# Optimization experiments

Measured on AMD Instinct MI355X. Metric: run time of the kernel, lower is better.

Reference implementation:

```python
import jax, jax.numpy as jnp
import numpy as np
import math

N_NODES = 50000
N_EDGES = 640000
IN_FEATS = 128
HEADS = 8
OUT_FEATS = 16
D_FF = 4 * IN_FEATS


def setup_inputs() -> dict:
    key = jax.random.key(0)
    ks = jax.random.split(key, 10)
    s = 0.05
    return {
        "feat": jax.random.normal(ks[0], (N_NODES, IN_FEATS), jnp.float32),
        "src": jax.random.randint(ks[1], (N_EDGES,), 0, N_NODES, jnp.int32),
        "dst": jax.random.randint(ks[2], (N_EDGES,), 0, N_NODES, jnp.int32),
        "Wq": jax.random.normal(ks[3], (IN_FEATS, HEADS * OUT_FEATS), jnp.float32) * s,
        "Wk": jax.random.normal(ks[4], (IN_FEATS, HEADS * OUT_FEATS), jnp.float32) * s,
        "Wv": jax.random.normal(ks[5], (IN_FEATS, HEADS * OUT_FEATS), jnp.float32) * s,
        "ln1_g": jnp.ones((IN_FEATS,), jnp.float32),
        "ln1_b": jnp.zeros((IN_FEATS,), jnp.float32),
        "W1": jax.random.normal(ks[6], (IN_FEATS, D_FF), jnp.float32) * s,
        "b1": jnp.zeros((D_FF,), jnp.float32),
        "prelu_a": jnp.full((D_FF,), 0.25, jnp.float32),  # torch PReLU default init
        "W2": jax.random.normal(ks[7], (D_FF, IN_FEATS), jnp.float32) * s,
        "b2": jnp.zeros((IN_FEATS,), jnp.float32),
    }


def layer_norm(x, g, b, eps=1e-5):
    mu = jnp.mean(x, axis=-1, keepdims=True)
    var = jnp.mean(jnp.square(x - mu), axis=-1, keepdims=True)
    return (x - mu) * jax.lax.rsqrt(var + eps) * g + b


def reference(feat, src, dst, Wq, Wk, Wv, ln1_g, ln1_b, W1, b1, prelu_a, W2, b2):
    N = feat.shape[0]
    feat_c = jax.lax.stop_gradient(feat)  # feat.clone().detach()
    q = (feat @ Wq).reshape(N, HEADS, OUT_FEATS)
    k = (feat_c @ Wk).reshape(N, HEADS, OUT_FEATS)
    v = (feat_c @ Wv).reshape(N, HEADS, OUT_FEATS)

    # edge score: dot(k[src], q[dst]) per head -> [E, H]
    e = jnp.einsum('ehd,ehd->eh', k[src], q[dst]) / math.sqrt(OUT_FEATS * HEADS)

    # segment softmax over incoming edges of each dst node
    m = jax.ops.segment_max(e, dst, num_segments=N)          # [N, H]
    e_exp = jnp.exp(e - m[dst])                              # [E, H]
    denom = jax.ops.segment_sum(e_exp, dst, num_segments=N)  # [N, H]
    a = e_exp / denom[dst]                                   # [E, H]

    # weighted scatter-sum aggregation
    msg = v[src] * a[:, :, None]                             # [E, H, D]
    ft2 = jax.ops.segment_sum(msg, dst, num_segments=N)      # [N, H, D]

    rst = ft2.reshape(feat.shape) + feat
    # NOTE: original applies ln1 twice (ln2 is unused) -- reproduced faithfully
    rst = layer_norm(rst, ln1_g, ln1_b)
    h = rst @ W1 + b1
    h = jnp.where(h >= 0, h, prelu_a * h)                    # PReLU, per-channel
    ffn = h @ W2 + b2
    rst = layer_norm(rst + ffn, ln1_g, ln1_b)
    return rst
```

## Files before the change

kernel.cpp:

```cpp
#include <hip/hip_runtime.h>

#define N_NODES 50000
#define N_EDGES 640000
#define F 128
#define DFF 512
#define NB 196

using u32 = unsigned int;
using u16 = unsigned short;

typedef __bf16 bf16x8 __attribute__((ext_vector_type(8)));
typedef float f32x4 __attribute__((ext_vector_type(4)));
typedef float f32x2 __attribute__((ext_vector_type(2)));

__device__ __forceinline__ float bf2f(u16 u) {
    return __uint_as_float(((u32)u) << 16);
}
__device__ __forceinline__ float blo(u32 p) { return __uint_as_float(p << 16); }
__device__ __forceinline__ float bhi(u32 p) { return __uint_as_float(p & 0xffff0000u); }
__device__ __forceinline__ u16 f2bf(float f) {
    u32 u = __float_as_uint(f);
    u += 0x7fffu + ((u >> 16) & 1u);
    return (u16)(u >> 16);
}
__device__ __forceinline__ u32 pack2(float a, float b) {
    return (u32)f2bf(a) | ((u32)f2bf(b) << 16);
}

#define FEAT_UNITS (N_NODES * F / 4)
#define PH_TOTAL (FEAT_UNITS + 180224 + N_EDGES)
__global__ void k_prep(const float* __restrict__ feat, u16* __restrict__ featb,
                       const float* __restrict__ Wq, const float* __restrict__ Wk,
                       const float* __restrict__ Wv, const float* __restrict__ W1,
                       const float* __restrict__ W2, u16* __restrict__ WT,
                       const int* __restrict__ dst, int* __restrict__ cnt) {
    int idx = blockIdx.x * 256 + threadIdx.x;
    if (idx < FEAT_UNITS) {
        float4 v = reinterpret_cast<const float4*>(feat)[idx];
        uint2 p;
        p.x = pack2(v.x, v.y);
        p.y = pack2(v.z, v.w);
        reinterpret_cast<uint2*>(featb)[idx] = p;
        return;
    }
    int wi = idx - FEAT_UNITS;
    if (wi < 180224) {
        if (wi < 49152) {
            int mi = wi >> 14;
            int local = wi & 16383;
            const float* W = (mi == 0) ? Wq : ((mi == 1) ? Wk : Wv);
            int n = local >> 7, k = local & 127;
            WT[wi] = f2bf(W[(size_t)k * 128 + n]);
        } else if (wi < 114688) {
            int local = wi - 49152;
            int n = local >> 7, k = local & 127;
            WT[wi] = f2bf(W1[(size_t)k * 512 + n]);
        } else {
            int local = wi - 114688;
            int n = local >> 9, k = local & 511;
            WT[wi] = f2bf(W2[(size_t)k * 128 + n]);
        }
        return;
    }
    int e = wi - 180224;
    if (e < N_EDGES) atomicAdd(&cnt[dst[e]], 1);
}

__global__ void k_bsum(const int* __restrict__ counts, int* __restrict__ bsum) {
    int i = blockIdx.x * 256 + threadIdx.x;
    int v = (i < N_NODES) ? counts[i] : 0;
#pragma unroll
    for (int off = 32; off >= 1; off >>= 1) v += __shfl_xor(v, off, 64);
    __shared__ int ws[4];
    int lane = threadIdx.x & 63, wid = threadIdx.x >> 6;
    if (lane == 0) ws[wid] = v;
    __syncthreads();
    if (threadIdx.x == 0) bsum[blockIdx.x] = ws[0] + ws[1] + ws[2] + ws[3];
}

__global__ void k_bfill(const int* __restrict__ counts, const int* __restrict__ bsum,
                        int* __restrict__ row_ptr) {
    int b = blockIdx.x, t = threadIdx.x;
    int lane = t & 63, wid = t >> 6;
    __shared__ int ws[4];
    __shared__ int sboff[256];

    int bv = (t < NB) ? bsum[t] : 0;
    int bincl = bv;
#pragma unroll
    for (int off = 1; off < 64; off <<= 1) {
        int u = __shfl_up(bincl, off, 64);
        if (lane >= off) bincl += u;
    }
    if (lane == 63) ws[wid] = bincl;
    __syncthreads();
    int bwo = 0;
#pragma unroll
    for (int j = 0; j < 4; ++j) if (j < wid) bwo += ws[j];
    sboff[t] = bwo + bincl - bv;
    __syncthreads();
    const int boff = sboff[b];

    int i = b * 256 + t;
    int v = (i < N_NODES) ? counts[i] : 0;
    int incl = v;
#pragma unroll
    for (int off = 1; off < 64; off <<= 1) {
        int u = __shfl_up(incl, off, 64);
        if (lane >= off) incl += u;
    }
    if (lane == 63) ws[wid] = incl;
    __syncthreads();
    int wo = 0;
#pragma unroll
    for (int j = 0; j < 4; ++j) if (j < wid) wo += ws[j];
    if (i < N_NODES) row_ptr[i] = boff + wo + incl - v;
    if (i == 0) row_ptr[N_NODES] = N_EDGES;
}

__global__ void k_fill(const int* __restrict__ src, const int* __restrict__ dst,
                       const int* __restrict__ row_ptr, int* __restrict__ fill,
                       int* __restrict__ csr_src) {
    int e = blockIdx.x * 256 + threadIdx.x;
    if (e < N_EDGES) {
        int d = dst[e];
        int pos = row_ptr[d] + atomicAdd(&fill[d], 1);
        csr_src[pos] = src[e];
    }
}

template <int EPI>
__global__ __launch_bounds__(256) void k_mm(
    const u16* __restrict__ A, int lda,
    const u16* __restrict__ BT,
    void* __restrict__ Cv, int ldc,
    int K,
    const float* __restrict__ bias,
    const float* __restrict__ prelu,
    const u16* __restrict__ resid,
    const float* __restrict__ g,
    const float* __restrict__ bb)
{
    __shared__ u16 smem[17408];
    u16* sA = smem;
    u16* sB = smem + 128 * 64;
    u16* sC = smem;

    const int t = threadIdx.x;
    const int w = t >> 6;
    const int lane = t & 63;
    const int ln = lane & 15, q4 = lane >> 4;
    const int row0 = blockIdx.x * 128;
    const int cb = blockIdx.y * 128;

    f32x4 acc[2][8];
#pragma unroll
    for (int mt = 0; mt < 2; ++mt)
#pragma unroll
        for (int nt = 0; nt < 8; ++nt)
            acc[mt][nt] = (f32x4){0.f, 0.f, 0.f, 0.f};

    uint4 pa[4], pb[4];
#define LOAD_A(kc)                                                             \
    {                                                                          \
        _Pragma("unroll") for (int i = 0; i < 4; ++i) {                        \
            int u = i * 256 + t, r = u >> 3, k8 = (u & 7) * 8;                 \
            int row = row0 + r;                                                \
            uint4 val = make_uint4(0, 0, 0, 0);                                \
            if (row < N_NODES)                                                 \
                val = *reinterpret_cast<const uint4*>(A + (size_t)row * lda + (kc) + k8); \
            pa[i] = val;                                                       \
        }                                                                      \
    }
#define LOAD_B(kc)                                                             \
    {                                                                          \
        _Pragma("unroll") for (int i = 0; i < 4; ++i) {                        \
            int u = i * 256 + t, r = u >> 3, k8 = (u & 7) * 8;                 \
            pb[i] = *reinterpret_cast<const uint4*>(BT + (size_t)(cb + r) * K + (kc) + k8); \
        }                                                                      \
    }

    LOAD_A(0);
    LOAD_B(0);

    for (int kc = 0; kc < K; kc += 64) {
#pragma unroll
        for (int i = 0; i < 4; ++i) {
            int u = i * 256 + t, r = u >> 3, gi = u & 7;
            int off = (r * 8 + (gi ^ (r & 7))) * 8;
            *reinterpret_cast<uint4*>(&sA[off]) = pa[i];
            *reinterpret_cast<uint4*>(&sB[off]) = pb[i];
        }
        __syncthreads();
        if (kc + 64 < K) {
            LOAD_A(kc + 64);
            LOAD_B(kc + 64);
        }
#pragma unroll
        for (int ks = 0; ks < 2; ++ks) {
            const int gsw = ks * 4 + q4;
            const int rA0 = w * 32 + ln;
            const int rA1 = rA0 + 16;
            bf16x8 a0 = *reinterpret_cast<const bf16x8*>(&sA[(rA0 * 8 + (gsw ^ (rA0 & 7))) * 8]);
            bf16x8 a1 = *reinterpret_cast<const bf16x8*>(&sA[(rA1 * 8 + (gsw ^ (rA1 & 7))) * 8]);
#pragma unroll
            for (int nt = 0; nt < 8; ++nt) {
                const int rB = nt * 16 + ln;
                bf16x8 b = *reinterpret_cast<const bf16x8*>(&sB[(rB * 8 + (gsw ^ (rB & 7))) * 8]);
                acc[0][nt] = __builtin_amdgcn_mfma_f32_16x16x32_bf16(a0, b, acc[0][nt], 0, 0, 0);
                acc[1][nt] = __builtin_amdgcn_mfma_f32_16x16x32_bf16(a1, b, acc[1][nt], 0, 0, 0);
            }
        }
        __syncthreads();
    }
#undef LOAD_A
#undef LOAD_B

    if (EPI == 0 || EPI == 1) {
        float bs[8], pr[8];
        if (EPI == 1) {
#pragma unroll
            for (int nt = 0; nt < 8; ++nt) {
                int col = cb + nt * 16 + ln;
                bs[nt] = bias[col];
                pr[nt] = prelu[col];
            }
        }
#pragma unroll
        for (int mt = 0; mt < 2; ++mt)
#pragma unroll
            for (int nt = 0; nt < 8; ++nt)
#pragma unroll
                for (int j = 0; j < 4; ++j) {
                    float x = acc[mt][nt][j];
                    if (EPI == 1) {
                        x += bs[nt];
                        x = (x >= 0.f) ? x : pr[nt] * x;
                    }
                    sC[(w * 32 + mt * 16 + q4 * 4 + j) * 136 + nt * 16 + ln] = f2bf(x);
                }
        __syncthreads();
        if (EPI == 0 && cb != 0) {
            u16* C = (u16*)Cv;
            const u32 vflag = (cb == 256) ? 1u : 0u;
#pragma unroll
            for (int i = 0; i < 32; ++i) {
                int u = i * 256 + t;
                int r = u >> 6, p = u & 63;
                int row = row0 + r;
                if (row < N_NODES) {
                    u32 pair = *reinterpret_cast<const u32*>(&sC[r * 136 + p * 2]);
                    int packed = __builtin_amdgcn_cvt_pk_fp8_f32(blo(pair), bhi(pair), 0, false);
                    C[(u32)row * 256u + 128u + (u32)p * 2u + vflag] = (u16)(packed & 0xffff);
                }
            }
        } else {
            u16* C = (u16*)Cv;
#pragma unroll
            for (int i = 0; i < 8; ++i) {
                int u = i * 256 + t;
                int r = u >> 4, c8 = (u & 15) * 8;
                int row = row0 + r;
                if (row < N_NODES) {
                    uint4 val = *reinterpret_cast<const uint4*>(&sC[r * 136 + c8]);
                    *reinterpret_cast<uint4*>(&C[(size_t)row * ldc + cb + c8]) = val;
                }
            }
        }
    } else {
        float* C = (float*)Cv;
        float bs[8], gv[8], bv[8];
#pragma unroll
        for (int nt = 0; nt < 8; ++nt) {
            int col = nt * 16 + ln;
            bs[nt] = bias[col];
            gv[nt] = g[col];
            bv[nt] = bb[col];
        }
#pragma unroll
        for (int mt = 0; mt < 2; ++mt)
#pragma unroll
            for (int j = 0; j < 4; ++j) {
                int row = row0 + w * 32 + mt * 16 + q4 * 4 + j;
                bool ok = row < N_NODES;
                float vals[8];
                float s = 0.f, ss = 0.f;
#pragma unroll
                for (int nt = 0; nt < 8; ++nt) {
                    float x = acc[mt][nt][j] + bs[nt];
                    if (ok) x += bf2f(resid[(size_t)row * 128 + nt * 16 + ln]);
                    vals[nt] = x;
                    s += x; ss += x * x;
                }
                s += __shfl_xor(s, 8, 16); ss += __shfl_xor(ss, 8, 16);
                s += __shfl_xor(s, 4, 16); ss += __shfl_xor(ss, 4, 16);
                s += __shfl_xor(s, 2, 16); ss += __shfl_xor(ss, 2, 16);
                s += __shfl_xor(s, 1, 16); ss += __shfl_xor(ss, 1, 16);
                float mu = s * (1.f / 128.f);
                float var = ss * (1.f / 128.f) - mu * mu;
                float rs = rsqrtf(var + 1e-5f);
                if (ok) {
#pragma unroll
                    for (int nt = 0; nt < 8; ++nt)
                        C[(size_t)row * 128 + nt * 16 + ln] =
                            (vals[nt] - mu) * rs * gv[nt] + bv[nt];
                }
            }
    }
}

__global__ __launch_bounds__(256) void k_attn(
    const u32* __restrict__ Q32, const float* __restrict__ feat,
    const int* __restrict__ row_ptr, const int* __restrict__ csr_src,
    const float* __restrict__ g, const float* __restrict__ bb,
    u16* __restrict__ rstb)
{
    const int w = threadIdx.x >> 6;
    const int lane = threadIdx.x & 63;
    const int n = blockIdx.x * 4 + w;
    if (n >= N_NODES) return;
    const float scale = 0.08838834764831845f;

    const u32 qp = Q32[(u32)n * 128u + (u32)lane];
    const float q0 = blo(qp), q1 = bhi(qp);
    const int e0 = row_ptr[n], e1 = row_ptr[n + 1];
    const u32 kvlane = 64u + (u32)lane;

    float l = 0.f, a0 = 0.f, a1 = 0.f;

#define LD4(S, KV)                                                                      \
    {                                                                                   \
        KV[0] = Q32[(u32)(S).x * 128u + kvlane];                                        \
        KV[1] = Q32[(u32)(S).y * 128u + kvlane];                                        \
        KV[2] = Q32[(u32)(S).z * 128u + kvlane];                                        \
        KV[3] = Q32[(u32)(S).w * 128u + kvlane];                                        \
    }
#define CG(KV)                                                                          \
    {                                                                                   \
        f32x2 k0 = __builtin_amdgcn_cvt_pk_f32_fp8((int)KV[0], false);                  \
        f32x2 k1 = __builtin_amdgcn_cvt_pk_f32_fp8((int)KV[1], false);                  \
        f32x2 k2 = __builtin_amdgcn_cvt_pk_f32_fp8((int)KV[2], false);                  \
        f32x2 k3 = __builtin_amdgcn_cvt_pk_f32_fp8((int)KV[3], false);                  \
        float p0 = k0.x * q0 + k0.y * q1;                                               \
        float p1 = k1.x * q0 + k1.y * q1;                                               \
        float p2 = k2.x * q0 + k2.y * q1;                                               \
        float p3 = k3.x * q0 + k3.y * q1;                                               \
        p0 += __shfl_xor(p0, 4, 8); p1 += __shfl_xor(p1, 4, 8);                         \
        p2 += __shfl_xor(p2, 4, 8); p3 += __shfl_xor(p3, 4, 8);                         \
        p0 += __shfl_xor(p0, 2, 8); p1 += __shfl_xor(p1, 2, 8);                         \
        p2 += __shfl_xor(p2, 2, 8); p3 += __shfl_xor(p3, 2, 8);                         \
        p0 += __shfl_xor(p0, 1, 8); p1 += __shfl_xor(p1, 1, 8);                         \
        p2 += __shfl_xor(p2, 1, 8); p3 += __shfl_xor(p3, 1, 8);                         \
        float ea = __expf(p0 * scale), eb = __expf(p1 * scale);                         \
        float ec = __expf(p2 * scale), ed = __expf(p3 * scale);                         \
        l += (ea + eb) + (ec + ed);                                                     \
        f32x2 v0 = __builtin_amdgcn_cvt_pk_f32_fp8((int)KV[0], true);                   \
        f32x2 v1 = __builtin_amdgcn_cvt_pk_f32_fp8((int)KV[1], true);                   \
        f32x2 v2 = __builtin_amdgcn_cvt_pk_f32_fp8((int)KV[2], true);                   \
        f32x2 v3 = __builtin_amdgcn_cvt_pk_f32_fp8((int)KV[3], true);                   \
        a0 += ea * v0.x + eb * v1.x + ec * v2.x + ed * v3.x;                            \
        a1 += ea * v0.y + eb * v1.y + ec * v2.y + ed * v3.y;                            \
    }

    int e = e0;
    int rem = e1 - e0;
    {
        int4 sA, sB;
        u32 kvA[4], kvB[4];
        if (rem >= 4) {
            sA = *reinterpret_cast<const int4*>(csr_src + e);
            LD4(sA, kvA);
            if (rem >= 8) {
                sB = *reinterpret_cast<const int4*>(csr_src + e + 4);
                while (true) {
                    if (rem >= 12) sA = *reinterpret_cast<const int4*>(csr_src + e + 8);
                    LD4(sB, kvB);
                    CG(kvA);
                    e += 4; rem -= 4;
                    if (rem < 8) { CG(kvB); e += 4; rem -= 4; break; }
                    if (rem >= 12) sB = *reinterpret_cast<const int4*>(csr_src + e + 8);
                    LD4(sA, kvA);
                    CG(kvB);
                    e += 4; rem -= 4;
                    if (rem < 8) { CG(kvA); e += 4; rem -= 4; break; }
                }
            } else {
                CG(kvA);
                e += 4; rem -= 4;
            }
        }
    }
    for (; e < e1; ++e) {
        int s0 = csr_src[e];
        u32 kv = Q32[(u32)s0 * 128u + kvlane];
        f32x2 kf = __builtin_amdgcn_cvt_pk_f32_fp8((int)kv, false);
        float p0 = kf.x * q0 + kf.y * q1;
        p0 += __shfl_xor(p0, 4, 8);
        p0 += __shfl_xor(p0, 2, 8);
        p0 += __shfl_xor(p0, 1, 8);
        float ea = __expf(p0 * scale);
        f32x2 vf = __builtin_amdgcn_cvt_pk_f32_fp8((int)kv, true);
        l += ea;
        a0 += ea * vf.x;
        a1 += ea * vf.y;
    }
#undef LD4
#undef CG

    float inv = (l > 0.f) ? 1.f / l : 0.f;
    const int c2 = lane * 2;
    const float2 fr = *reinterpret_cast<const float2*>(feat + (size_t)n * 128 + c2);
    float x0 = a0 * inv + fr.x;
    float x1 = a1 * inv + fr.y;

    float sum = x0 + x1, sq = x0 * x0 + x1 * x1;
#pragma unroll
    for (int off = 32; off >= 1; off >>= 1) {
        sum += __shfl_xor(sum, off, 64);
        sq += __shfl_xor(sq, off, 64);
    }
    float mu = sum * (1.f / 128.f);
    float var = sq * (1.f / 128.f) - mu * mu;
    float rs = rsqrtf(var + 1e-5f);
    float y0 = (x0 - mu) * rs * g[c2] + bb[c2];
    float y1 = (x1 - mu) * rs * g[c2 + 1] + bb[c2 + 1];
    reinterpret_cast<u32*>(rstb)[(size_t)n * 64 + lane] = pack2(y0, y1);
}

extern "C" void kernel_launch(void* const* d_in, const int* in_sizes, int n_in,
                              void* d_out, int out_size, void* d_ws, size_t ws_size,
                              hipStream_t stream)
{
    const float* feat = (const float*)d_in[0];
    const int* src    = (const int*)d_in[1];
    const int* dst    = (const int*)d_in[2];
    const float* Wq   = (const float*)d_in[3];
    const float* Wk   = (const float*)d_in[4];
    const float* Wv   = (const float*)d_in[5];
    const float* ln_g = (const float*)d_in[6];
    const float* ln_b = (const float*)d_in[7];
    const float* W1   = (const float*)d_in[8];
    const float* b1   = (const float*)d_in[9];
    const float* pa   = (const float*)d_in[10];
    const float* W2   = (const float*)d_in[11];
    const float* b2   = (const float*)d_in[12];

    u16* qkv   = (u16*)d_ws;
    u16* h     = qkv + (size_t)N_NODES * 384;
    u16* featb = h;
    u16* rstb  = h + (size_t)N_NODES * 512;
    u16* WT    = rstb + (size_t)N_NODES * 128;
    u16* BqkvT = WT;
    u16* W1T   = WT + 49152;
    u16* W2T   = WT + 114688;
    int* counts  = (int*)(WT + 180224);
    int* fill    = counts + N_NODES;
    int* row_ptr = fill + N_NODES;
    int* csr_src = row_ptr + N_NODES + 1;
    int* bsum    = csr_src + N_EDGES;

    hipMemsetAsync(counts, 0, sizeof(int) * 2 * N_NODES, stream);
    k_prep<<<(PH_TOTAL + 255) / 256, 256, 0, stream>>>(
        feat, featb, Wq, Wk, Wv, W1, W2, WT, dst, counts);

    k_bsum<<<NB, 256, 0, stream>>>(counts, bsum);
    k_bfill<<<NB, 256, 0, stream>>>(counts, bsum, row_ptr);
    k_fill<<<(N_EDGES + 255) / 256, 256, 0, stream>>>(src, dst, row_ptr, fill, csr_src);

    const int MBK = (N_NODES + 127) / 128;

    dim3 gqkv(MBK, 3);
    k_mm<0><<<gqkv, 256, 0, stream>>>(featb, 128, BqkvT, qkv, 256, 128,
                                      nullptr, nullptr, nullptr, nullptr, nullptr);

    k_attn<<<(N_NODES + 3) / 4, 256, 0, stream>>>((const u32*)qkv, feat, row_ptr, csr_src,
                                                  ln_g, ln_b, rstb);

    dim3 gf1(MBK, 4);
    k_mm<1><<<gf1, 256, 0, stream>>>(rstb, 128, W1T, h, 512, 128,
                                     b1, pa, nullptr, nullptr, nullptr);

    dim3 gf2(MBK, 1);
    k_mm<2><<<gf2, 256, 0, stream>>>(h, 512, W2T, d_out, 128, 512,
                                     b2, nullptr, rstb, ln_g, ln_b);
}
```

Baseline: 304.2 us.

## Fuse FFN GEMMs into one kernel keeping hidden activations in shared memory

```diff
diff --git a/kernel.cpp b/kernel.cpp
--- a/kernel.cpp
+++ b/kernel.cpp
@@ -216,16 +216,7 @@
 #undef LOAD_A
 #undef LOAD_B
 
-    if (EPI == 0 || EPI == 1) {
-        float bs[8], pr[8];
-        if (EPI == 1) {
-#pragma unroll
-            for (int nt = 0; nt < 8; ++nt) {
-                int col = cb + nt * 16 + ln;
-                bs[nt] = bias[col];
-                pr[nt] = prelu[col];
-            }
-        }
+    {
 #pragma unroll
         for (int mt = 0; mt < 2; ++mt)
 #pragma unroll
@@ -233,10 +224,6 @@
 #pragma unroll
                 for (int j = 0; j < 4; ++j) {
                     float x = acc[mt][nt][j];
-                    if (EPI == 1) {
-                        x += bs[nt];
-                        x = (x >= 0.f) ? x : pr[nt] * x;
-                    }
                     sC[(w * 32 + mt * 16 + q4 * 4 + j) * 136 + nt * 16 + ln] = f2bf(x);
                 }
         __syncthreads();
@@ -267,46 +254,141 @@
                 }
             }
         }
-    } else {
-        float* C = (float*)Cv;
-        float bs[8], gv[8], bv[8];
-#pragma unroll
-        for (int nt = 0; nt < 8; ++nt) {
-            int col = nt * 16 + ln;
-            bs[nt] = bias[col];
-            gv[nt] = g[col];
-            bv[nt] = bb[col];
-        }
+    }
+}
+
+__global__ __launch_bounds__(256) void k_ffn(
+    const u16* __restrict__ rstb,
+    const u16* __restrict__ W1T,
+    const u16* __restrict__ W2T,
+    const float* __restrict__ b1,
+    const float* __restrict__ prelu,
+    const float* __restrict__ b2,
+    const float* __restrict__ g,
+    const float* __restrict__ bb,
+    float* __restrict__ out)
+{
+    __shared__ u16 sA[16384];
+    __shared__ u16 sH[16384];
+
+    const int t = threadIdx.x;
+    const int w = t >> 6;
+    const int lane = t & 63;
+    const int ln = lane & 15, q4 = lane >> 4;
+    const int row0 = blockIdx.x * 128;
+
+#pragma unroll
+    for (int i = 0; i < 8; ++i) {
+        int u = i * 256 + t, r = u >> 4, gi = u & 15;
+        int row = row0 + r;
+        uint4 val = make_uint4(0, 0, 0, 0);
+        if (row < N_NODES)
+            val = *reinterpret_cast<const uint4*>(rstb + (size_t)row * 128 + gi * 8);
+        *reinterpret_cast<uint4*>(&sA[(r * 16 + (gi ^ (r & 15))) * 8]) = val;
+    }
+    __syncthreads();
+
+    const int rA0 = w * 32 + ln;
+    const int rA1 = rA0 + 16;
+
+    f32x4 acc2[2][8];
+#pragma unroll
+    for (int mt = 0; mt < 2; ++mt)
+#pragma unroll
+        for (int nt = 0; nt < 8; ++nt)
+            acc2[mt][nt] = (f32x4){0.f, 0.f, 0.f, 0.f};
+
+    for (int c = 0; c < 4; ++c) {
+        f32x4 acc1[2][8];
 #pragma unroll
         for (int mt = 0; mt < 2; ++mt)
 #pragma unroll
-            for (int j = 0; j < 4; ++j) {
-                int row = row0 + w * 32 + mt * 16 + q4 * 4 + j;
-                bool ok = row < N_NODES;
-                float vals[8];
-                float s = 0.f, ss = 0.f;
-#pragma unroll
-                for (int nt = 0; nt < 8; ++nt) {
-                    float x = acc[mt][nt][j] + bs[nt];
-                    if (ok) x += bf2f(resid[(size_t)row * 128 + nt * 16 + ln]);
-                    vals[nt] = x;
-                    s += x; ss += x * x;
+            for (int nt = 0; nt < 8; ++nt)
+                acc1[mt][nt] = (f32x4){0.f, 0.f, 0.f, 0.f};
+#pragma unroll
+        for (int ks = 0; ks < 4; ++ks) {
+            const int gsw = ks * 4 + q4;
+            bf16x8 a0 = *reinterpret_cast<const bf16x8*>(&sA[(rA0 * 16 + (gsw ^ (rA0 & 15))) * 8]);
+            bf16x8 a1 = *reinterpret_cast<const bf16x8*>(&sA[(rA1 * 16 + (gsw ^ (rA1 & 15))) * 8]);
+#pragma unroll
+            for (int nt = 0; nt < 8; ++nt) {
+                bf16x8 b = *reinterpret_cast<const bf16x8*>(
+                    W1T + (size_t)(c * 128 + nt * 16 + ln) * 128 + ks * 32 + q4 * 8);
+                acc1[0][nt] = __builtin_amdgcn_mfma_f32_16x16x32_bf16(a0, b, acc1[0][nt], 0, 0, 0);
+                acc1[1][nt] = __builtin_amdgcn_mfma_f32_16x16x32_bf16(a1, b, acc1[1][nt], 0, 0, 0);
+            }
+        }
+#pragma unroll
+        for (int mt = 0; mt < 2; ++mt)
+#pragma unroll
+            for (int nt = 0; nt < 8; ++nt) {
+                const int col = nt * 16 + ln;
+                const float bsv = b1[c * 128 + col];
+                const float prv = prelu[c * 128 + col];
+                const int gi = col >> 3;
+#pragma unroll
+                for (int j = 0; j < 4; ++j) {
+                    float x = acc1[mt][nt][j] + bsv;
+                    x = (x >= 0.f) ? x : prv * x;
+                    const int row = w * 32 + mt * 16 + q4 * 4 + j;
+                    sH[(row * 16 + (gi ^ (row & 15))) * 8 + (col & 7)] = f2bf(x);
                 }
-                s += __shfl_xor(s, 8, 16); ss += __shfl_xor(ss, 8, 16);
-                s += __shfl_xor(s, 4, 16); ss += __shfl_xor(ss, 4, 16);
-                s += __shfl_xor(s, 2, 16); ss += __shfl_xor(ss, 2, 16);
-                s += __shfl_xor(s, 1, 16); ss += __shfl_xor(ss, 1, 16);
-                float mu = s * (1.f / 128.f);
-                float var = ss * (1.f / 128.f) - mu * mu;
-                float rs = rsqrtf(var + 1e-5f);
-                if (ok) {
-#pragma unroll
-                    for (int nt = 0; nt < 8; ++nt)
-                        C[(size_t)row * 128 + nt * 16 + ln] =
-                            (vals[nt] - mu) * rs * gv[nt] + bv[nt];
-                }
-            }
-    }
+            }
+#pragma unroll
+        for (int ks = 0; ks < 4; ++ks) {
+            const int gsw = ks * 4 + q4;
+            bf16x8 h0 = *reinterpret_cast<const bf16x8*>(&sH[(rA0 * 16 + (gsw ^ (rA0 & 15))) * 8]);
+            bf16x8 h1 = *reinterpret_cast<const bf16x8*>(&sH[(rA1 * 16 + (gsw ^ (rA1 & 15))) * 8]);
+#pragma unroll
+            for (int nt = 0; nt < 8; ++nt) {
+                bf16x8 b = *reinterpret_cast<const bf16x8*>(
+                    W2T + (size_t)(nt * 16 + ln) * 512 + c * 128 + ks * 32 + q4 * 8);
+                acc2[0][nt] = __builtin_amdgcn_mfma_f32_16x16x32_bf16(h0, b, acc2[0][nt], 0, 0, 0);
+                acc2[1][nt] = __builtin_amdgcn_mfma_f32_16x16x32_bf16(h1, b, acc2[1][nt], 0, 0, 0);
+            }
+        }
+    }
+
+    float bs[8], gv[8], bv[8];
+#pragma unroll
+    for (int nt = 0; nt < 8; ++nt) {
+        int col = nt * 16 + ln;
+        bs[nt] = b2[col];
+        gv[nt] = g[col];
+        bv[nt] = bb[col];
+    }
+#pragma unroll
+    for (int mt = 0; mt < 2; ++mt)
+#pragma unroll
+        for (int j = 0; j < 4; ++j) {
+            const int lrow = w * 32 + mt * 16 + q4 * 4 + j;
+            const int row = row0 + lrow;
+            const bool ok = row < N_NODES;
+            float vals[8];
+            float s = 0.f, ss = 0.f;
+#pragma unroll
+            for (int nt = 0; nt < 8; ++nt) {
+                const int col = nt * 16 + ln;
+                const int gi = col >> 3;
+                float res = bf2f(sA[(lrow * 16 + (gi ^ (lrow & 15))) * 8 + (col & 7)]);
+                float x = acc2[mt][nt][j] + bs[nt] + res;
+                vals[nt] = x;
+                s += x; ss += x * x;
+            }
+            s += __shfl_xor(s, 8, 16); ss += __shfl_xor(ss, 8, 16);
+            s += __shfl_xor(s, 4, 16); ss += __shfl_xor(ss, 4, 16);
+            s += __shfl_xor(s, 2, 16); ss += __shfl_xor(ss, 2, 16);
+            s += __shfl_xor(s, 1, 16); ss += __shfl_xor(ss, 1, 16);
+            float mu = s * (1.f / 128.f);
+            float var = ss * (1.f / 128.f) - mu * mu;
+            float rs = rsqrtf(var + 1e-5f);
+            if (ok) {
+#pragma unroll
+                for (int nt = 0; nt < 8; ++nt)
+                    out[(size_t)row * 128 + nt * 16 + ln] =
+                        (vals[nt] - mu) * rs * gv[nt] + bv[nt];
+            }
+        }
 }
 
 __global__ __launch_bounds__(256) void k_attn(
@@ -476,11 +558,6 @@
     k_attn<<<(N_NODES + 3) / 4, 256, 0, stream>>>((const u32*)qkv, feat, row_ptr, csr_src,
                                                   ln_g, ln_b, rstb);
 
-    dim3 gf1(MBK, 4);
-    k_mm<1><<<gf1, 256, 0, stream>>>(rstb, 128, W1T, h, 512, 128,
-                                     b1, pa, nullptr, nullptr, nullptr);
-
-    dim3 gf2(MBK, 1);
-    k_mm<2><<<gf2, 256, 0, stream>>>(h, 512, W2T, d_out, 128, 512,
-                                     b2, nullptr, rstb, ln_g, ln_b);
-}
+    k_ffn<<<MBK, 256, 0, stream>>>(rstb, W1T, W2T, b1, pa, b2, ln_g, ln_b,
+                                   (float*)d_out);
+}
```

Result: slower. 363.1 us (+19.4%).
